# Optimization experiments

Measured on AMD Instinct MI355X. Metric: run time of the kernel, lower is better.

Reference implementation:

```python
import jax, jax.numpy as jnp
import numpy as np

N, E, F, H, L, G = 100000, 1600000, 32, 64, 4, 256
EPS = 1e-5


def setup_inputs() -> dict:
    key = jax.random.key(0)
    ks = jax.random.split(key, 12)
    x = jax.random.normal(ks[0], (N, F), dtype=jnp.float32)
    edge_index = jax.random.randint(ks[1], (2, E), 0, N, dtype=jnp.int32)
    batch = jnp.sort(jax.random.randint(ks[2], (N,), 0, G, dtype=jnp.int32))
    s = 0.1
    return {
        "x": x,
        "edge_index": edge_index,
        "batch": batch,
        "w_embed": jax.random.normal(ks[3], (F, H), dtype=jnp.float32) * s,
        "b_embed": jnp.zeros((H,), dtype=jnp.float32),
        "conv_W": jax.random.normal(ks[4], (L, H, H), dtype=jnp.float32) * s,
        "conv_b": jnp.zeros((L, H), dtype=jnp.float32),
        "bn_gamma": jnp.ones((L, H), dtype=jnp.float32),
        "bn_beta": jnp.zeros((L, H), dtype=jnp.float32),
        "w1": jax.random.normal(ks[5], (H, H // 2), dtype=jnp.float32) * s,
        "b1": jnp.zeros((H // 2,), dtype=jnp.float32),
        "w2": jax.random.normal(ks[6], (H // 2, 1), dtype=jnp.float32) * s,
        "b2": jnp.zeros((1,), dtype=jnp.float32),
    }


def _gcn_conv(h, src, dst, W, b):
    # PyG GCNConv: add self loops, symmetric D^-1/2 (A+I) D^-1/2 normalization
    hw = h @ W  # [N,H]
    deg = jax.ops.segment_sum(jnp.ones((E,), h.dtype), dst, num_segments=N) + 1.0
    dinv = jax.lax.rsqrt(deg)  # [N]
    msg = hw[src] * (dinv[src] * dinv[dst])[:, None]  # [E,H] gather + scale
    agg = jax.ops.segment_sum(msg, dst, num_segments=N)  # scatter-add
    agg = agg + hw * (dinv * dinv)[:, None]  # self-loop contribution
    return agg + b


def _batchnorm(h, gamma, beta):
    # training-mode BatchNorm1d over the node dimension
    mean = jnp.mean(h, axis=0)
    var = jnp.var(h, axis=0)
    return (h - mean) * jax.lax.rsqrt(var + EPS) * gamma + beta


def reference(x, edge_index, batch, w_embed, b_embed, conv_W, conv_b,
              bn_gamma, bn_beta, w1, b1, w2, b2):
    src, dst = edge_index[0], edge_index[1]
    h = x @ w_embed + b_embed  # node embedding [N,H]
    for i in range(L):
        identity = h
        h = _gcn_conv(h, src, dst, conv_W[i], conv_b[i])
        h = _batchnorm(h, bn_gamma[i], bn_beta[i])
        h = jax.nn.relu(h)
        # dropout is identity in eval mode
        h = h + identity  # use_residual=True
    # global mean pool over graphs
    sums = jax.ops.segment_sum(h, batch, num_segments=G)  # [G,H]
    counts = jax.ops.segment_sum(jnp.ones((N,), h.dtype), batch, num_segments=G)
    pooled = sums / jnp.maximum(counts, 1.0)[:, None]
    out = jax.nn.relu(pooled @ w1 + b1)
    out = out @ w2 + b2  # [G,1]
    return out
```

## Files before the change

### kernel.cpp

```cpp
#include <hip/hip_runtime.h>
#include <hip/hip_fp16.h>

#define Nn 100000
#define Ne 1600000
#define Fi 32
#define Hd 64
#define Ll 4
#define Gg 256
#define BN_EPS 1e-5f
#define NPB 128
#define NBINS ((Nn + NPB - 1) / NPB)
#define CHUNK 4096
#define NBLK ((Ne + CHUNK - 1) / CHUNK)
#define IDXW (NBINS + 2)
#define TPAD 68
#define XPAD 36
#define NGB ((Nn + 63) / 64)
#define NSH 128


__global__ void k_scanA(const int* __restrict__ deg, int* __restrict__ row_off,
                        int* __restrict__ bsum) {
    __shared__ int s[256];
    int t = threadIdx.x;
    int i = blockIdx.x * 256 + t;
    int v = (i < Nn) ? deg[i] : 0;
    s[t] = v;
    __syncthreads();
    int x = v;
    for (int off = 1; off < 256; off <<= 1) {
        int u = (t >= off) ? s[t - off] : 0;
        __syncthreads();
        x += u;
        s[t] = x;
        __syncthreads();
    }
    if (i < Nn) row_off[i] = x - v;
    if (t == 255) bsum[blockIdx.x] = x;
}

__global__ void k_scanBG(int* __restrict__ bsum, int nblk,
                         const int* __restrict__ batch, int* __restrict__ gstart) {
    int t = threadIdx.x;
    if (blockIdx.x == 1) {
        if (t < Gg) {
            int lo = 0, hi = Nn;
            while (lo < hi) {
                int mid = (lo + hi) >> 1;
                if (batch[mid] < t) lo = mid + 1; else hi = mid;
            }
            gstart[t] = lo;
            if (t == 0) gstart[Gg] = Nn;
        }
        return;
    }
    __shared__ int s[512];
    int v = (t < nblk) ? bsum[t] : 0;
    s[t] = v;
    __syncthreads();
    int x = v;
    for (int off = 1; off < 512; off <<= 1) {
        int u = (t >= off) ? s[t - off] : 0;
        __syncthreads();
        x += u;
        s[t] = x;
        __syncthreads();
    }
    if (t < nblk) bsum[t] = x - v;
}

__global__ void k_scanC(int* __restrict__ row_off, const int* __restrict__ bsum,
                        const int* __restrict__ deg, float* __restrict__ dinv) {
    int i = blockIdx.x * 256 + threadIdx.x;
    if (i < Nn) {
        row_off[i] += bsum[blockIdx.x];
        dinv[i] = rsqrtf((float)deg[i] + 1.0f);
    }
    if (i == 0) row_off[Nn] = Ne;
}

__global__ __launch_bounds__(256) void k_part(const int* __restrict__ src,
                                              const int* __restrict__ dst,
                                              unsigned* __restrict__ tpack,
                                              unsigned short* __restrict__ idx16) {
    __shared__ int hist[NBINS];
    __shared__ int lofs[NBINS + 1];
    __shared__ int wsum[256];
    __shared__ unsigned stage[CHUNK];
    int blk = blockIdx.x, t = threadIdx.x;
    int e0 = blk * CHUNK;
    int nval = min(CHUNK, Ne - e0);

    for (int i = t; i < NBINS; i += 256) hist[i] = 0;
    __syncthreads();
    for (int i = t; i < nval; i += 256)
        atomicAdd(&hist[dst[e0 + i] >> 7], 1);
    __syncthreads();

    int base = t * 4;
    int loc[4];
    int s = 0;
#pragma unroll
    for (int k = 0; k < 4; k++) {
        int b = base + k;
        int c = (b < NBINS) ? hist[b] : 0;
        loc[k] = s;
        s += c;
    }
    wsum[t] = s;
    __syncthreads();
    int x = s;
    for (int off = 1; off < 256; off <<= 1) {
        int u = (t >= off) ? wsum[t - off] : 0;
        __syncthreads();
        x += u;
        wsum[t] = x;
        __syncthreads();
    }
    int excl = x - s;
#pragma unroll
    for (int k = 0; k < 4; k++) {
        int b = base + k;
        if (b < NBINS) lofs[b] = excl + loc[k];
    }
    if (t == 0) lofs[NBINS] = nval;
    __syncthreads();

    for (int i = t; i <= NBINS; i += 256)
        idx16[(size_t)blk * IDXW + i] = (unsigned short)lofs[i];

    for (int i = t; i < NBINS; i += 256) hist[i] = lofs[i];
    __syncthreads();
    for (int i = t; i < nval; i += 256) {
        int d = dst[e0 + i];
        int sv = src[e0 + i];
        int p = atomicAdd(&hist[d >> 7], 1);
        stage[p] = (unsigned)sv | ((unsigned)(d & (NPB - 1)) << 17);
    }
    __syncthreads();
    for (int i = t; i < nval; i += 256)
        tpack[(size_t)blk * CHUNK + i] = stage[i];
}

__global__ __launch_bounds__(256) void k_deg2(const unsigned* __restrict__ tpack,
                                              const unsigned short* __restrict__ idx16,
                                              int* __restrict__ deg) {
    __shared__ int cnt[NPB];
    int b = blockIdx.x, t = threadIdx.x;
    if (t < NPB) cnt[t] = 0;
    __syncthreads();
    for (int r = t; r < NBLK; r += 256) {
        const unsigned short* row = idx16 + (size_t)r * IDXW;
        int s = row[b], e = row[b + 1];
        const unsigned* tp = tpack + (size_t)r * CHUNK;
        for (int k = s; k < e; k++)
            atomicAdd(&cnt[tp[k] >> 17], 1);
    }
    __syncthreads();
    int node = b * NPB + t;
    if (t < NPB && node < Nn) deg[node] = cnt[t];
}

__global__ __launch_bounds__(256) void k_csr(const int* __restrict__ row_off,
                                             const unsigned* __restrict__ tpack,
                                             const unsigned short* __restrict__ idx16,
                                             int* __restrict__ esrc) {
    __shared__ int cur[NPB];
    int b = blockIdx.x, t = threadIdx.x;
    int n0 = b * NPB;
    int e0 = row_off[n0];
    if (t < NPB) {
        int node = n0 + t;
        cur[t] = (node < Nn) ? (row_off[node] - e0) : 0;
    }
    __syncthreads();
    for (int r = t; r < NBLK; r += 256) {
        const unsigned short* row = idx16 + (size_t)r * IDXW;
        int s = row[b], e = row[b + 1];
        const unsigned* tp = tpack + (size_t)r * CHUNK;
        for (int k = s; k < e; k++) {
            unsigned v = tp[k];
            int p = atomicAdd(&cur[v >> 17], 1);
            esrc[e0 + p] = (int)(v & 0x1FFFFu);
        }
    }
}


#define MT_FMA(AV, W0, W1, W2, W3, R)                                          \
    acc[R][0] = fmaf(AV.x, W0.x, acc[R][0]);                                   \
    acc[R][0] = fmaf(AV.y, W1.x, acc[R][0]);                                   \
    acc[R][0] = fmaf(AV.z, W2.x, acc[R][0]);                                   \
    acc[R][0] = fmaf(AV.w, W3.x, acc[R][0]);                                   \
    acc[R][1] = fmaf(AV.x, W0.y, acc[R][1]);                                   \
    acc[R][1] = fmaf(AV.y, W1.y, acc[R][1]);                                   \
    acc[R][1] = fmaf(AV.z, W2.y, acc[R][1]);                                   \
    acc[R][1] = fmaf(AV.w, W3.y, acc[R][1]);                                   \
    acc[R][2] = fmaf(AV.x, W0.z, acc[R][2]);                                   \
    acc[R][2] = fmaf(AV.y, W1.z, acc[R][2]);                                   \
    acc[R][2] = fmaf(AV.z, W2.z, acc[R][2]);                                   \
    acc[R][2] = fmaf(AV.w, W3.z, acc[R][2]);                                   \
    acc[R][3] = fmaf(AV.x, W0.w, acc[R][3]);                                   \
    acc[R][3] = fmaf(AV.y, W1.w, acc[R][3]);                                   \
    acc[R][3] = fmaf(AV.z, W2.w, acc[R][3]);                                   \
    acc[R][3] = fmaf(AV.w, W3.w, acc[R][3]);

__device__ inline void store_half4(unsigned short* dst, float a, float b,
                                   float c, float d) {
    __half2 p0 = __floats2half2_rn(a, b);
    __half2 p1 = __floats2half2_rn(c, d);
    uint2 u;
    u.x = *(unsigned*)&p0;
    u.y = *(unsigned*)&p1;
    *(uint2*)dst = u;
}

__device__ inline void store_half8(unsigned short* dst, const float* a) {
    __half2 p0 = __floats2half2_rn(a[0], a[1]);
    __half2 p1 = __floats2half2_rn(a[2], a[3]);
    __half2 p2 = __floats2half2_rn(a[4], a[5]);
    __half2 p3 = __floats2half2_rn(a[6], a[7]);
    uint4 u;
    u.x = *(unsigned*)&p0; u.y = *(unsigned*)&p1;
    u.z = *(unsigned*)&p2; u.w = *(unsigned*)&p3;
    *(uint4*)dst = u;
}

__device__ inline float4 load_half4(const unsigned short* p) {
    uint2 u = *(const uint2*)p;
    float2 f0 = __half22float2(*(__half2*)&u.x);
    float2 f1 = __half22float2(*(__half2*)&u.y);
    return make_float4(f0.x, f0.y, f1.x, f1.y);
}

__global__ __launch_bounds__(256, 4) void k_gemmF2(const unsigned short* __restrict__ aggh,
                                                   const float* __restrict__ bnacc,
                                                   const float* __restrict__ gamma,
                                                   const float* __restrict__ beta,
                                                   unsigned short* __restrict__ hh,
                                                   const float* __restrict__ W,
                                                   const float* __restrict__ dinv,
                                                   unsigned short* __restrict__ hwh) {
    __shared__ float hs[64 * TPAD];
    __shared__ float ws[64 * 64];
    __shared__ float bsc[64], bsh[64];
    int t = threadIdx.x;
    int n0 = blockIdx.x * 64;

    for (int f = t; f < 1024; f += 256)
        ((float4*)ws)[f] = ((const float4*)W)[f];

    if (t < 64) {
        float s = 0.f, s2 = 0.f;
        for (int shd = 0; shd < NSH; shd++) {
            s  += bnacc[shd * 128 + t];
            s2 += bnacc[shd * 128 + 64 + t];
        }
        float mean = s / (float)Nn;
        float var = fmaxf(s2 / (float)Nn - mean * mean, 0.f);
        float scv = gamma[t] * rsqrtf(var + BN_EPS);
        bsc[t] = scv;
        bsh[t] = beta[t] - mean * scv;
    }
    __syncthreads();

    for (int f = t; f < 1024; f += 256) {
        int row = f >> 4, c4 = (f & 15) * 4;
        int node = n0 + row;
        if (node < Nn) {
            float4 a  = load_half4(aggh + (size_t)node * Hd + c4);
            float4 ho = load_half4(hh + (size_t)node * Hd + c4);
            float4 sc = ((const float4*)bsc)[f & 15];
            float4 sh = ((const float4*)bsh)[f & 15];
            float4 r4;
            r4.x = fmaxf(fmaf(a.x, sc.x, sh.x), 0.f) + ho.x;
            r4.y = fmaxf(fmaf(a.y, sc.y, sh.y), 0.f) + ho.y;
            r4.z = fmaxf(fmaf(a.z, sc.z, sh.z), 0.f) + ho.z;
            r4.w = fmaxf(fmaf(a.w, sc.w, sh.w), 0.f) + ho.w;
            store_half4(hh + (size_t)node * Hd + c4, r4.x, r4.y, r4.z, r4.w);
            *(float4*)&hs[row * TPAD + c4] = r4;
        } else {
            *(float4*)&hs[row * TPAD + c4] = make_float4(0.f, 0.f, 0.f, 0.f);
        }
    }
    __syncthreads();

    int i = t >> 4, j = t & 15;
    float acc[4][4] = {};
#pragma unroll 2
    for (int k = 0; k < 64; k += 4) {
        float4 w0 = *(const float4*)&ws[(k + 0) * 64 + 4 * j];
        float4 w1 = *(const float4*)&ws[(k + 1) * 64 + 4 * j];
        float4 w2 = *(const float4*)&ws[(k + 2) * 64 + 4 * j];
        float4 w3 = *(const float4*)&ws[(k + 3) * 64 + 4 * j];
        float4 a0 = *(const float4*)&hs[(4 * i + 0) * TPAD + k];
        float4 a1 = *(const float4*)&hs[(4 * i + 1) * TPAD + k];
        float4 a2 = *(const float4*)&hs[(4 * i + 2) * TPAD + k];
        float4 a3 = *(const float4*)&hs[(4 * i + 3) * TPAD + k];
        MT_FMA(a0, w0, w1, w2, w3, 0)
        MT_FMA(a1, w0, w1, w2, w3, 1)
        MT_FMA(a2, w0, w1, w2, w3, 2)
        MT_FMA(a3, w0, w1, w2, w3, 3)
    }
#pragma unroll
    for (int r = 0; r < 4; r++) {
        int node = n0 + 4 * i + r;
        if (node < Nn) {
            float dv = dinv[node];
            store_half4(hwh + (size_t)node * Hd + 4 * j,
                        acc[r][0] * dv, acc[r][1] * dv, acc[r][2] * dv,
                        acc[r][3] * dv);
        }
    }
}

__global__ __launch_bounds__(256, 4) void k_embed_gemm2(const float* __restrict__ x,
                                                        const float* __restrict__ we,
                                                        const float* __restrict__ be,
                                                        const float* __restrict__ W,
                                                        unsigned short* __restrict__ hh,
                                                        const float* __restrict__ dinv,
                                                        unsigned short* __restrict__ hwh) {
    __shared__ float uni[64 * XPAD + 32 * 64];
    __shared__ float hs[64 * TPAD];
    __shared__ float bes[64];
    float* xs  = uni;
    float* wes = uni + 64 * XPAD;
    float* ws  = uni;
    int t = threadIdx.x;
    int n0 = blockIdx.x * 64;

    for (int f = t; f < 512; f += 256)
        ((float4*)wes)[f] = ((const float4*)we)[f];
    if (t < 64) bes[t] = be[t];

    for (int f = t; f < 512; f += 256) {
        int row = f >> 3, c4 = (f & 7) * 4;
        int node = n0 + row;
        float4 v = (node < Nn) ? *(const float4*)(x + (size_t)node * Fi + c4)
                               : make_float4(0.f, 0.f, 0.f, 0.f);
        *(float4*)&xs[row * XPAD + c4] = v;
    }
    __syncthreads();

    int i = t >> 4, j = t & 15;
    {
        float acc[4][4];
#pragma unroll
        for (int r = 0; r < 4; r++)
#pragma unroll
            for (int c = 0; c < 4; c++) acc[r][c] = bes[4 * j + c];
#pragma unroll 2
        for (int k = 0; k < 32; k += 4) {
            float4 w0 = *(const float4*)&wes[(k + 0) * 64 + 4 * j];
            float4 w1 = *(const float4*)&wes[(k + 1) * 64 + 4 * j];
            float4 w2 = *(const float4*)&wes[(k + 2) * 64 + 4 * j];
            float4 w3 = *(const float4*)&wes[(k + 3) * 64 + 4 * j];
            float4 a0 = *(const float4*)&xs[(4 * i + 0) * XPAD + k];
            float4 a1 = *(const float4*)&xs[(4 * i + 1) * XPAD + k];
            float4 a2 = *(const float4*)&xs[(4 * i + 2) * XPAD + k];
            float4 a3 = *(const float4*)&xs[(4 * i + 3) * XPAD + k];
            MT_FMA(a0, w0, w1, w2, w3, 0)
            MT_FMA(a1, w0, w1, w2, w3, 1)
            MT_FMA(a2, w0, w1, w2, w3, 2)
            MT_FMA(a3, w0, w1, w2, w3, 3)
        }
#pragma unroll
        for (int r = 0; r < 4; r++) {
            int node = n0 + 4 * i + r;
            float4 hv = make_float4(acc[r][0], acc[r][1], acc[r][2], acc[r][3]);
            *(float4*)&hs[(4 * i + r) * TPAD + 4 * j] = hv;
            if (node < Nn)
                store_half4(hh + (size_t)node * Hd + 4 * j, hv.x, hv.y, hv.z, hv.w);
        }
    }
    __syncthreads();
    for (int f = t; f < 1024; f += 256)
        ((float4*)ws)[f] = ((const float4*)W)[f];
    __syncthreads();
    {
        float acc[4][4] = {};
#pragma unroll 2
        for (int k = 0; k < 64; k += 4) {
            float4 w0 = *(const float4*)&ws[(k + 0) * 64 + 4 * j];
            float4 w1 = *(const float4*)&ws[(k + 1) * 64 + 4 * j];
            float4 w2 = *(const float4*)&ws[(k + 2) * 64 + 4 * j];
            float4 w3 = *(const float4*)&ws[(k + 3) * 64 + 4 * j];
            float4 a0 = *(const float4*)&hs[(4 * i + 0) * TPAD + k];
            float4 a1 = *(const float4*)&hs[(4 * i + 1) * TPAD + k];
            float4 a2 = *(const float4*)&hs[(4 * i + 2) * TPAD + k];
            float4 a3 = *(const float4*)&hs[(4 * i + 3) * TPAD + k];
            MT_FMA(a0, w0, w1, w2, w3, 0)
            MT_FMA(a1, w0, w1, w2, w3, 1)
            MT_FMA(a2, w0, w1, w2, w3, 2)
            MT_FMA(a3, w0, w1, w2, w3, 3)
        }
#pragma unroll
        for (int r = 0; r < 4; r++) {
            int node = n0 + 4 * i + r;
            if (node < Nn) {
                float dv = dinv[node];
                store_half4(hwh + (size_t)node * Hd + 4 * j,
                            acc[r][0] * dv, acc[r][1] * dv, acc[r][2] * dv,
                            acc[r][3] * dv);
            }
        }
    }
}


__global__ __launch_bounds__(256) void k_gatherH(const unsigned short* __restrict__ hwh,
                                                 const float* __restrict__ dinv,
                                                 const int* __restrict__ row_off,
                                                 const int* __restrict__ esrc,
                                                 const float* __restrict__ bias,
                                                 unsigned short* __restrict__ aggh,
                                                 float* __restrict__ bnacc) {
    int g = threadIdx.x >> 3;
    int l = threadIdx.x & 7;
    int node = blockIdx.x * 32 + g;
    float di = dinv[node];
    float acc[8];

    uint4 v = *(const uint4*)(hwh + (size_t)node * Hd + l * 8);
#pragma unroll
    for (int q = 0; q < 4; q++) {
        float2 f = __half22float2(*(__half2*)(((unsigned*)&v) + q));
        acc[2 * q]     = f.x;
        acc[2 * q + 1] = f.y;
    }

    int e = row_off[node], e1 = row_off[node + 1];
    for (; e + 7 < e1; e += 8) {
        uint4 vv[8];
#pragma unroll
        for (int u = 0; u < 8; u++)
            vv[u] = *(const uint4*)(hwh + (size_t)esrc[e + u] * Hd + l * 8);
#pragma unroll
        for (int u = 0; u < 8; u++) {
#pragma unroll
            for (int q = 0; q < 4; q++) {
                float2 f = __half22float2(*(__half2*)(((unsigned*)&vv[u]) + q));
                acc[2 * q]     += f.x;
                acc[2 * q + 1] += f.y;
            }
        }
    }
    for (; e + 1 < e1; e += 2) {
        uint4 v0 = *(const uint4*)(hwh + (size_t)esrc[e] * Hd + l * 8);
        uint4 v1 = *(const uint4*)(hwh + (size_t)esrc[e + 1] * Hd + l * 8);
#pragma unroll
        for (int q = 0; q < 4; q++) {
            float2 f0 = __half22float2(*(__half2*)(((unsigned*)&v0) + q));
            float2 f1 = __half22float2(*(__half2*)(((unsigned*)&v1) + q));
            acc[2 * q]     += f0.x + f1.x;
            acc[2 * q + 1] += f0.y + f1.y;
        }
    }
    if (e < e1) {
        uint4 v0 = *(const uint4*)(hwh + (size_t)esrc[e] * Hd + l * 8);
#pragma unroll
        for (int q = 0; q < 4; q++) {
            float2 f0 = __half22float2(*(__half2*)(((unsigned*)&v0) + q));
            acc[2 * q]     += f0.x;
            acc[2 * q + 1] += f0.y;
        }
    }

#pragma unroll
    for (int q = 0; q < 8; q++)
        acc[q] = fmaf(acc[q], di, bias[l * 8 + q]);

    store_half8(aggh + (size_t)node * Hd + l * 8, acc);

    __shared__ float ls[2048];
    *(float4*)&ls[g * 64 + l * 8]     = make_float4(acc[0], acc[1], acc[2], acc[3]);
    *(float4*)&ls[g * 64 + l * 8 + 4] = make_float4(acc[4], acc[5], acc[6], acc[7]);
    __syncthreads();
    int t = threadIdx.x;
    if (t < 64) {
        float s = 0.f, s2 = 0.f;
#pragma unroll
        for (int gg = 0; gg < 32; gg++) {
            float vv = ls[gg * 64 + t];
            s += vv;
            s2 = fmaf(vv, vv, s2);
        }
        float* a = bnacc + (blockIdx.x & (NSH - 1)) * 128;
        atomicAdd(&a[t], s);
        atomicAdd(&a[64 + t], s2);
    }
}

__global__ __launch_bounds__(1024) void k_poolF(const unsigned short* __restrict__ aggh,
                                                const float* __restrict__ bnacc,
                                                const float* __restrict__ gamma,
                                                const float* __restrict__ beta,
                                                const unsigned short* __restrict__ hh,
                                                const int* __restrict__ gstart,
                                                float* __restrict__ pooled) {
    __shared__ float ls[1024];
    __shared__ float bsc[64], bsh[64];
    int g = blockIdx.x;
    int t = threadIdx.x;
    if (t < 64) {
        float s = 0.f, s2 = 0.f;
        for (int shd = 0; shd < NSH; shd++) {
            s  += bnacc[shd * 128 + t];
            s2 += bnacc[shd * 128 + 64 + t];
        }
        float mean = s / (float)Nn;
        float var = fmaxf(s2 / (float)Nn - mean * mean, 0.f);
        float scv = gamma[t] * rsqrtf(var + BN_EPS);
        bsc[t] = scv;
        bsh[t] = beta[t] - mean * scv;
    }
    __syncthreads();
    int ch = t & 63, sl = t >> 6;
    float sc = bsc[ch], shv = bsh[ch];
    int n0 = gstart[g], n1 = gstart[g + 1];
    float s = 0.f;
    for (int n = n0 + sl; n < n1; n += 16) {
        float a  = __half2float(((const __half*)aggh)[(size_t)n * Hd + ch]);
        float ho = __half2float(((const __half*)hh)[(size_t)n * Hd + ch]);
        s += fmaxf(fmaf(a, sc, shv), 0.f) + ho;
    }
    ls[t] = s;
    __syncthreads();
    if (t < 64) {
        float acc = 0.f;
#pragma unroll
        for (int k = 0; k < 16; k++) acc += ls[k * 64 + t];
        float cnt = (float)(n1 - n0);
        pooled[g * Hd + t] = acc / fmaxf(cnt, 1.0f);
    }
}

__global__ __launch_bounds__(256) void k_head(const float* __restrict__ pooled,
                                              const float* __restrict__ w1,
                                              const float* __restrict__ b1,
                                              const float* __restrict__ w2,
                                              const float* __restrict__ b2,
                                              float* __restrict__ out) {
    __shared__ float sw1[Hd * 32], sw2[32], sb1[32];
    int t = threadIdx.x;
    for (int i = t; i < Hd * 32; i += 256) sw1[i] = w1[i];
    if (t < 32) { sw2[t] = w2[t]; sb1[t] = b1[t]; }
    __syncthreads();
    float acc2[32];
#pragma unroll
    for (int k = 0; k < 32; k++) acc2[k] = sb1[k];
    for (int j = 0; j < Hd; j++) {
        float pj = pooled[t * Hd + j];
#pragma unroll
        for (int k = 0; k < 32; k++) acc2[k] = fmaf(pj, sw1[j * 32 + k], acc2[k]);
    }
    float o = b2[0];
#pragma unroll
    for (int k = 0; k < 32; k++) o += fmaxf(acc2[k], 0.f) * sw2[k];
    out[t] = o;
}


extern "C" void kernel_launch(void* const* d_in, const int* in_sizes, int n_in,
                              void* d_out, int out_size, void* d_ws, size_t ws_size,
                              hipStream_t stream) {
    const float* x       = (const float*)d_in[0];
    const int*   eidx    = (const int*)d_in[1];
    const int*   batch   = (const int*)d_in[2];
    const float* w_embed = (const float*)d_in[3];
    const float* b_embed = (const float*)d_in[4];
    const float* conv_W  = (const float*)d_in[5];
    const float* conv_b  = (const float*)d_in[6];
    const float* gamma   = (const float*)d_in[7];
    const float* beta    = (const float*)d_in[8];
    const float* w1      = (const float*)d_in[9];
    const float* b1      = (const float*)d_in[10];
    const float* w2      = (const float*)d_in[11];
    const float* b2      = (const float*)d_in[12];
    const int* src = eidx;
    const int* dst = eidx + Ne;

    char* p = (char*)d_ws;
    auto alloc = [&](size_t bytes) -> void* {
        void* r = (void*)p;
        p += (bytes + 255) / 256 * 256;
        return r;
    };
    unsigned short* hh  = (unsigned short*)alloc((size_t)Nn * Hd * 2);
    unsigned short* hwh = (unsigned short*)alloc((size_t)Nn * Hd * 2);
    unsigned short* aggh = (unsigned short*)alloc((size_t)Nn * Hd * 2);
    int*      deg     = (int*)alloc((size_t)Nn * 4);
    int*      row_off = (int*)alloc((size_t)(Nn + 1) * 4);
    float*    dinv    = (float*)alloc((size_t)Nn * 4);
    int*      bsum    = (int*)alloc(512 * 4);
    int*      esrc    = (int*)alloc((size_t)Ne * 4);
    unsigned* tpack   = (unsigned*)alloc((size_t)NBLK * CHUNK * 4);
    unsigned short* idx16 = (unsigned short*)alloc((size_t)NBLK * IDXW * 2);
    float*    bnacc   = (float*)alloc((size_t)Ll * NSH * 128 * 4);
    float*    pooled  = (float*)alloc((size_t)Gg * Hd * 4);
    int*      gstart  = (int*)alloc((size_t)(Gg + 1) * 4);
    (void)ws_size; (void)in_sizes; (void)n_in; (void)out_size;

    const int NB_N = (Nn + 255) / 256;
    const int NB_G32 = Nn / 32;

    hipMemsetAsync(bnacc, 0, (size_t)Ll * NSH * 128 * 4, stream);

    k_part<<<NBLK, 256, 0, stream>>>(src, dst, tpack, idx16);
    k_deg2<<<NBINS, 256, 0, stream>>>(tpack, idx16, deg);
    k_scanA<<<NB_N, 256, 0, stream>>>(deg, row_off, bsum);
    k_scanBG<<<2, 512, 0, stream>>>(bsum, NB_N, batch, gstart);
    k_scanC<<<NB_N, 256, 0, stream>>>(row_off, bsum, deg, dinv);
    k_csr<<<NBINS, 256, 0, stream>>>(row_off, tpack, idx16, esrc);

    k_embed_gemm2<<<NGB, 256, 0, stream>>>(x, w_embed, b_embed, conv_W, hh, dinv, hwh);

    for (int i = 0; i < Ll; i++) {
        if (i > 0)
            k_gemmF2<<<NGB, 256, 0, stream>>>(aggh, bnacc + (size_t)(i - 1) * NSH * 128,
                                              gamma + (size_t)(i - 1) * Hd,
                                              beta + (size_t)(i - 1) * Hd, hh,
                                              conv_W + (size_t)i * Hd * Hd, dinv, hwh);
        k_gatherH<<<NB_G32, 256, 0, stream>>>(hwh, dinv, row_off, esrc,
                                              conv_b + (size_t)i * Hd, aggh,
                                              bnacc + (size_t)i * NSH * 128);
    }

    k_poolF<<<Gg, 1024, 0, stream>>>(aggh, bnacc + (size_t)(Ll - 1) * NSH * 128,
                                     gamma + (size_t)(Ll - 1) * Hd,
                                     beta + (size_t)(Ll - 1) * Hd, hh, gstart, pooled);
    k_head<<<1, 256, 0, stream>>>(pooled, w1, b1, w2, b2, (float*)d_out);
}
```

Before: 326.5 us.

## Fuse degree count, scans and CSR build into one padded-slot kernel

Replaces the degree kernel, three scan kernels and the CSR scatter kernel with a single kernel. Each 128-node bin gets a fixed 4096-entry slot in esrc, so no global prefix scan is needed. Each block loads its bin's edges into shared memory, counts and scans locally, writes row_off, degree and dinv, then writes its sorted sources out contiguously. This removes four launches and repeated global reads of tpack, at the cost of a padded esrc layout, an extra rdeg read in the gather kernel, and an assumption that no bin holds more than 4096 edges.

```diff
diff --git a/kernel.cpp b/kernel.cpp
--- a/kernel.cpp
+++ b/kernel.cpp
@@ -13,71 +13,12 @@
 #define CHUNK 4096
 #define NBLK ((Ne + CHUNK - 1) / CHUNK)
 #define IDXW (NBINS + 2)
+#define BSLOT 4096
 #define TPAD 68
 #define XPAD 36
 #define NGB ((Nn + 63) / 64)
 #define NSH 128
 
-
-__global__ void k_scanA(const int* __restrict__ deg, int* __restrict__ row_off,
-                        int* __restrict__ bsum) {
-    __shared__ int s[256];
-    int t = threadIdx.x;
-    int i = blockIdx.x * 256 + t;
-    int v = (i < Nn) ? deg[i] : 0;
-    s[t] = v;
-    __syncthreads();
-    int x = v;
-    for (int off = 1; off < 256; off <<= 1) {
-        int u = (t >= off) ? s[t - off] : 0;
-        __syncthreads();
-        x += u;
-        s[t] = x;
-        __syncthreads();
-    }
-    if (i < Nn) row_off[i] = x - v;
-    if (t == 255) bsum[blockIdx.x] = x;
-}
-
-__global__ void k_scanBG(int* __restrict__ bsum, int nblk,
-                         const int* __restrict__ batch, int* __restrict__ gstart) {
-    int t = threadIdx.x;
-    if (blockIdx.x == 1) {
-        if (t < Gg) {
-            int lo = 0, hi = Nn;
-            while (lo < hi) {
-                int mid = (lo + hi) >> 1;
-                if (batch[mid] < t) lo = mid + 1; else hi = mid;
-            }
-            gstart[t] = lo;
-            if (t == 0) gstart[Gg] = Nn;
-        }
-        return;
-    }
-    __shared__ int s[512];
-    int v = (t < nblk) ? bsum[t] : 0;
-    s[t] = v;
-    __syncthreads();
-    int x = v;
-    for (int off = 1; off < 512; off <<= 1) {
-        int u = (t >= off) ? s[t - off] : 0;
-        __syncthreads();
-        x += u;
-        s[t] = x;
-        __syncthreads();
-    }
-    if (t < nblk) bsum[t] = x - v;
-}
-
-__global__ void k_scanC(int* __restrict__ row_off, const int* __restrict__ bsum,
-                        const int* __restrict__ deg, float* __restrict__ dinv) {
-    int i = blockIdx.x * 256 + threadIdx.x;
-    if (i < Nn) {
-        row_off[i] += bsum[blockIdx.x];
-        dinv[i] = rsqrtf((float)deg[i] + 1.0f);
-    }
-    if (i == 0) row_off[Nn] = Ne;
-}
 
 __global__ __launch_bounds__(256) void k_part(const int* __restrict__ src,
                                               const int* __restrict__ dst,
@@ -142,48 +83,90 @@
         tpack[(size_t)blk * CHUNK + i] = stage[i];
 }
 
-__global__ __launch_bounds__(256) void k_deg2(const unsigned* __restrict__ tpack,
+__global__ __launch_bounds__(512) void k_csr2(const unsigned* __restrict__ tpack,
                                               const unsigned short* __restrict__ idx16,
-                                              int* __restrict__ deg) {
-    __shared__ int cnt[NPB];
-    int b = blockIdx.x, t = threadIdx.x;
+                                              const int* __restrict__ batch,
+                                              int* __restrict__ esrc,
+                                              int* __restrict__ row_off,
+                                              int* __restrict__ rdeg,
+                                              float* __restrict__ dinv,
+                                              int* __restrict__ gstart) {
+    int t = threadIdx.x;
+    if (blockIdx.x == NBINS) {
+        if (t < Gg) {
+            int lo = 0, hi = Nn;
+            while (lo < hi) {
+                int mid = (lo + hi) >> 1;
+                if (batch[mid] < t) lo = mid + 1; else hi = mid;
+            }
+            gstart[t] = lo;
+            if (t == 0) gstart[Gg] = Nn;
+        }
+        return;
+    }
+    __shared__ unsigned edges[BSLOT];
+    __shared__ unsigned ordered[BSLOT];
+    __shared__ int rlen[512];
+    __shared__ int cnt[NPB], startv[NPB], cur[NPB];
+    int b = blockIdx.x;
+    int n0 = b * NPB;
+    int base = b * BSLOT;
+
+    int len = 0, s0 = 0;
+    if (t < NBLK) {
+        const unsigned short* row = idx16 + (size_t)t * IDXW;
+        s0 = row[b];
+        len = (int)row[b + 1] - s0;
+    }
+    rlen[t] = len;
+    __syncthreads();
+    int x = len;
+    for (int off = 1; off < 512; off <<= 1) {
+        int u = (t >= off) ? rlen[t - off] : 0;
+        __syncthreads();
+        x += u;
+        rlen[t] = x;
+        __syncthreads();
+    }
+    int lput = x - len;
+    int total = rlen[511];
+    if (t < NBLK && len > 0) {
+        const unsigned* tp = tpack + (size_t)t * CHUNK + s0;
+        for (int k = 0; k < len; k++)
+            edges[lput + k] = tp[k];
+    }
     if (t < NPB) cnt[t] = 0;
     __syncthreads();
-    for (int r = t; r < NBLK; r += 256) {
-        const unsigned short* row = idx16 + (size_t)r * IDXW;
-        int s = row[b], e = row[b + 1];
-        const unsigned* tp = tpack + (size_t)r * CHUNK;
-        for (int k = s; k < e; k++)
-            atomicAdd(&cnt[tp[k] >> 17], 1);
-    }
-    __syncthreads();
-    int node = b * NPB + t;
-    if (t < NPB && node < Nn) deg[node] = cnt[t];
-}
-
-__global__ __launch_bounds__(256) void k_csr(const int* __restrict__ row_off,
-                                             const unsigned* __restrict__ tpack,
-                                             const unsigned short* __restrict__ idx16,
-                                             int* __restrict__ esrc) {
-    __shared__ int cur[NPB];
-    int b = blockIdx.x, t = threadIdx.x;
-    int n0 = b * NPB;
-    int e0 = row_off[n0];
+    for (int i = t; i < total; i += 512)
+        atomicAdd(&cnt[edges[i] >> 17], 1);
+    __syncthreads();
+    if (t < NPB) startv[t] = cnt[t];
+    __syncthreads();
+    for (int off = 1; off < NPB; off <<= 1) {
+        int u = (t < NPB && t >= off) ? startv[t - off] : 0;
+        __syncthreads();
+        if (t < NPB) startv[t] += u;
+        __syncthreads();
+    }
     if (t < NPB) {
+        int st = startv[t] - cnt[t];
+        cur[t] = st;
         int node = n0 + t;
-        cur[t] = (node < Nn) ? (row_off[node] - e0) : 0;
-    }
-    __syncthreads();
-    for (int r = t; r < NBLK; r += 256) {
-        const unsigned short* row = idx16 + (size_t)r * IDXW;
-        int s = row[b], e = row[b + 1];
-        const unsigned* tp = tpack + (size_t)r * CHUNK;
-        for (int k = s; k < e; k++) {
-            unsigned v = tp[k];
-            int p = atomicAdd(&cur[v >> 17], 1);
-            esrc[e0 + p] = (int)(v & 0x1FFFFu);
-        }
-    }
+        if (node < Nn) {
+            row_off[node] = base + st;
+            rdeg[node] = cnt[t];
+            dinv[node] = rsqrtf((float)cnt[t] + 1.0f);
+        }
+    }
+    __syncthreads();
+    for (int i = t; i < total; i += 512) {
+        unsigned v = edges[i];
+        int p = atomicAdd(&cur[v >> 17], 1);
+        ordered[p] = v & 0x1FFFFu;
+    }
+    __syncthreads();
+    for (int i = t; i < total; i += 512)
+        esrc[base + i] = (int)ordered[i];
 }
 
 
@@ -412,6 +395,7 @@
 __global__ __launch_bounds__(256) void k_gatherH(const unsigned short* __restrict__ hwh,
                                                  const float* __restrict__ dinv,
                                                  const int* __restrict__ row_off,
+                                                 const int* __restrict__ rdeg,
                                                  const int* __restrict__ esrc,
                                                  const float* __restrict__ bias,
                                                  unsigned short* __restrict__ aggh,
@@ -430,7 +414,8 @@
         acc[2 * q + 1] = f.y;
     }
 
-    int e = row_off[node], e1 = row_off[node + 1];
+    int e = row_off[node];
+    int e1 = e + rdeg[node];
     for (; e + 7 < e1; e += 8) {
         uint4 vv[8];
 #pragma unroll
@@ -590,11 +575,10 @@
     unsigned short* hh  = (unsigned short*)alloc((size_t)Nn * Hd * 2);
     unsigned short* hwh = (unsigned short*)alloc((size_t)Nn * Hd * 2);
     unsigned short* aggh = (unsigned short*)alloc((size_t)Nn * Hd * 2);
-    int*      deg     = (int*)alloc((size_t)Nn * 4);
-    int*      row_off = (int*)alloc((size_t)(Nn + 1) * 4);
+    int*      row_off = (int*)alloc((size_t)Nn * 4);
+    int*      rdeg    = (int*)alloc((size_t)Nn * 4);
     float*    dinv    = (float*)alloc((size_t)Nn * 4);
-    int*      bsum    = (int*)alloc(512 * 4);
-    int*      esrc    = (int*)alloc((size_t)Ne * 4);
+    int*      esrc    = (int*)alloc((size_t)NBINS * BSLOT * 4);
     unsigned* tpack   = (unsigned*)alloc((size_t)NBLK * CHUNK * 4);
     unsigned short* idx16 = (unsigned short*)alloc((size_t)NBLK * IDXW * 2);
     float*    bnacc   = (float*)alloc((size_t)Ll * NSH * 128 * 4);
@@ -602,17 +586,13 @@
     int*      gstart  = (int*)alloc((size_t)(Gg + 1) * 4);
     (void)ws_size; (void)in_sizes; (void)n_in; (void)out_size;
 
-    const int NB_N = (Nn + 255) / 256;
     const int NB_G32 = Nn / 32;
 
     hipMemsetAsync(bnacc, 0, (size_t)Ll * NSH * 128 * 4, stream);
 
     k_part<<<NBLK, 256, 0, stream>>>(src, dst, tpack, idx16);
-    k_deg2<<<NBINS, 256, 0, stream>>>(tpack, idx16, deg);
-    k_scanA<<<NB_N, 256, 0, stream>>>(deg, row_off, bsum);
-    k_scanBG<<<2, 512, 0, stream>>>(bsum, NB_N, batch, gstart);
-    k_scanC<<<NB_N, 256, 0, stream>>>(row_off, bsum, deg, dinv);
-    k_csr<<<NBINS, 256, 0, stream>>>(row_off, tpack, idx16, esrc);
+    k_csr2<<<NBINS + 1, 512, 0, stream>>>(tpack, idx16, batch, esrc, row_off,
+                                          rdeg, dinv, gstart);
 
     k_embed_gemm2<<<NGB, 256, 0, stream>>>(x, w_embed, b_embed, conv_W, hh, dinv, hwh);
 
@@ -622,7 +602,7 @@
                                               gamma + (size_t)(i - 1) * Hd,
                                               beta + (size_t)(i - 1) * Hd, hh,
                                               conv_W + (size_t)i * Hd * Hd, dinv, hwh);
-        k_gatherH<<<NB_G32, 256, 0, stream>>>(hwh, dinv, row_off, esrc,
+        k_gatherH<<<NB_G32, 256, 0, stream>>>(hwh, dinv, row_off, rdeg, esrc,
                                               conv_b + (size_t)i * Hd, aggh,
                                               bnacc + (size_t)i * NSH * 128);
     }
```

Result: faster. 293.6 us (median of 2 runs) (-10.1%).
